# Kernel tuning notes

Measured on AMD Instinct MI355X. Metric: run time of the kernel, lower is better.

The kernel has to match this reference:

```python
import jax, jax.numpy as jnp
import numpy as np

B, H, S, D = 2, 8, 2048, 64


def setup_inputs() -> dict:
    key = jax.random.key(0)
    kq, kk, kv, km = jax.random.split(key, 4)
    Q = jax.random.normal(kq, (B, H, S, D), dtype=jnp.float32)
    K = jax.random.normal(kk, (B, H, S, D), dtype=jnp.float32)
    V = jax.random.normal(kv, (B, H, S, D), dtype=jnp.float32)
    attn_mask = jax.random.bernoulli(km, p=0.1, shape=(B, H, S, S))
    return {"Q": Q, "K": K, "V": V, "attn_mask": attn_mask, "d_k": D}


def reference(Q, K, V, attn_mask, d_k):
    # scores = Q K^T / sqrt(d_k)  -> [B,H,S,S]
    scale = 1.0 / np.sqrt(d_k).astype(np.float32)
    scores = jnp.einsum("bhqd,bhkd->bhqk", Q, K) * scale
    scores = jnp.where(attn_mask, jnp.float32(-1e9), scores)
    attn = jax.nn.softmax(scores, axis=-1)
    # dropout is identity in eval mode (deterministic reference)
    context = jnp.einsum("bhqk,bhkd->bhqd", attn, V)
    return (context, attn)
```

## Files before the change

kernel.cpp:

```cpp
#include <hip/hip_runtime.h>
#include <stdint.h>

#define S_LEN 2048
#define D_HEAD 64
#define NBH 16
#define NROWS (NBH * S_LEN)
#define CTX_ELEMS (NBH * S_LEN * D_HEAD)


__global__ void detect_mask_kernel(const uint32_t* __restrict__ m, int* flag) {
  __shared__ int any;
  if (threadIdx.x == 0) any = 0;
  __syncthreads();
  int local = 0;
  for (int i = threadIdx.x; i < 16384; i += 256)
    if (m[i] > 1u) local = 1;
  if (local) atomicOr(&any, 1);
  __syncthreads();
  if (threadIdx.x == 0) *flag = any;
}

__global__ __launch_bounds__(256, 3) void qk_exp_kernel(
    const float* __restrict__ Q, const float* __restrict__ K,
    const void* __restrict__ mask, float* __restrict__ e_out,
    float* __restrict__ psum, const int* __restrict__ mflag) {
  __shared__ float Qs[32][132];
  __shared__ float Ks[32][132];
  const int bh = blockIdx.z;
  const int mBase = blockIdx.y * 128;
  const int nBase = blockIdx.x * 128;
  const float* __restrict__ Qb = Q + (size_t)bh * S_LEN * D_HEAD;
  const float* __restrict__ Kb = K + (size_t)bh * S_LEN * D_HEAD;
  float* __restrict__ Eb = e_out + (size_t)bh * S_LEN * S_LEN;
  const int tid = threadIdx.x;
  const int maskIsBytes = *mflag;

  const int ty = (tid >> 4) << 3;
  const int cj = (tid & 15) << 2;
  float acc[8][8] = {};

#pragma unroll
  for (int ph = 0; ph < 2; ++ph) {
    const int dBase = ph * 32;
    if (ph) __syncthreads();
#pragma unroll
    for (int i = 0; i < 4; ++i) {
      const int f4 = tid + i * 256;
      const int row = f4 >> 3;
      const int d0 = (f4 & 7) << 2;
      const float4 qv = *reinterpret_cast<const float4*>(
          Qb + (size_t)(mBase + row) * D_HEAD + dBase + d0);
      const float4 kv = *reinterpret_cast<const float4*>(
          Kb + (size_t)(nBase + row) * D_HEAD + dBase + d0);
      Qs[d0 + 0][row] = qv.x; Qs[d0 + 1][row] = qv.y;
      Qs[d0 + 2][row] = qv.z; Qs[d0 + 3][row] = qv.w;
      Ks[d0 + 0][row] = kv.x; Ks[d0 + 1][row] = kv.y;
      Ks[d0 + 2][row] = kv.z; Ks[d0 + 3][row] = kv.w;
    }
    __syncthreads();
#pragma unroll 4
    for (int d = 0; d < 32; ++d) {
      const float4 q0 = *reinterpret_cast<const float4*>(&Qs[d][ty]);
      const float4 q1 = *reinterpret_cast<const float4*>(&Qs[d][ty + 4]);
      const float4 kl = *reinterpret_cast<const float4*>(&Ks[d][cj]);
      const float4 kh = *reinterpret_cast<const float4*>(&Ks[d][64 + cj]);
      const float qv[8] = {q0.x, q0.y, q0.z, q0.w, q1.x, q1.y, q1.z, q1.w};
      const float kv[8] = {kl.x, kl.y, kl.z, kl.w, kh.x, kh.y, kh.z, kh.w};
#pragma unroll
      for (int i = 0; i < 8; ++i)
#pragma unroll
        for (int j = 0; j < 8; ++j)
          acc[i][j] = fmaf(qv[i], kv[j], acc[i][j]);
    }
  }

  const float scale = 0.125f;
#pragma unroll
  for (int i = 0; i < 8; ++i) {
    const int row = mBase + ty + i;
    float e[8];
    if (maskIsBytes) {
      const unsigned char* mrow =
          (const unsigned char*)mask + ((size_t)bh * S_LEN + row) * S_LEN;
      const uint32_t ml = *reinterpret_cast<const uint32_t*>(mrow + nBase + cj);
      const uint32_t mh =
          *reinterpret_cast<const uint32_t*>(mrow + nBase + 64 + cj);
#pragma unroll
      for (int j = 0; j < 4; ++j) {
        e[j] = ((ml >> (8 * j)) & 0xffu) ? 0.0f : __expf(acc[i][j] * scale);
        e[4 + j] =
            ((mh >> (8 * j)) & 0xffu) ? 0.0f : __expf(acc[i][4 + j] * scale);
      }
    } else {
      const int* mrow = (const int*)mask + ((size_t)bh * S_LEN + row) * S_LEN;
      const int4 m0 = *reinterpret_cast<const int4*>(mrow + nBase + cj);
      const int4 m1 = *reinterpret_cast<const int4*>(mrow + nBase + 64 + cj);
      const int mi[8] = {m0.x, m0.y, m0.z, m0.w, m1.x, m1.y, m1.z, m1.w};
#pragma unroll
      for (int j = 0; j < 8; ++j)
        e[j] = mi[j] ? 0.0f : __expf(acc[i][j] * scale);
    }
    const float4 o0 = {e[0], e[1], e[2], e[3]};
    const float4 o1 = {e[4], e[5], e[6], e[7]};
    float* dst = Eb + (size_t)row * S_LEN + nBase;
    *reinterpret_cast<float4*>(dst + cj) = o0;
    *reinterpret_cast<float4*>(dst + 64 + cj) = o1;

    float r = (e[0] + e[1] + e[2] + e[3]) + (e[4] + e[5] + e[6] + e[7]);
    r += __shfl_xor(r, 1, 64);
    r += __shfl_xor(r, 2, 64);
    r += __shfl_xor(r, 4, 64);
    r += __shfl_xor(r, 8, 64);
    if ((tid & 15) == 0)
      psum[((size_t)bh * S_LEN + row) * 16 + blockIdx.x] = r;
  }
}

__global__ __launch_bounds__(256) void row_inv_kernel(
    const float* __restrict__ psum, float* __restrict__ inv) {
  const int row = blockIdx.x * 256 + threadIdx.x;
  const float4* p = reinterpret_cast<const float4*>(psum + (size_t)row * 16);
  const float4 a = p[0], b = p[1], c = p[2], d = p[3];
  const float s = ((a.x + a.y) + (a.z + a.w)) + ((b.x + b.y) + (b.z + b.w)) +
                  ((c.x + c.y) + (c.z + c.w)) + ((d.x + d.y) + (d.z + d.w));
  inv[row] = 1.0f / s;
}

__global__ __launch_bounds__(256, 4) void pv_kernel(
    float* __restrict__ attn, const float* __restrict__ V,
    const float* __restrict__ inv, float* __restrict__ part, int kLen) {
  __shared__ float Es[32][132];
  __shared__ float Vs[32][68];
  __shared__ float inv_s[128];
  const int bh = blockIdx.y;
  const int mBase = blockIdx.x * 128;
  const int z = blockIdx.z;
  float* __restrict__ Ab = attn + (size_t)bh * S_LEN * S_LEN;
  const float* __restrict__ Vb = V + (size_t)bh * S_LEN * D_HEAD;
  float* __restrict__ outb =
      part + (size_t)z * CTX_ELEMS + (size_t)bh * S_LEN * D_HEAD;
  const int tid = threadIdx.x;

  if (tid < 128) inv_s[tid] = inv[(size_t)bh * S_LEN + mBase + tid];

  const int ty = (tid >> 4) << 3;
  const int tx = (tid & 15) << 2;
  float acc[8][4] = {};
  const int kBeg = z * kLen;
  for (int kt = kBeg; kt < kBeg + kLen; kt += 32) {
    __syncthreads();
#pragma unroll
    for (int j = 0; j < 4; ++j) {
      const int f4 = tid + j * 256;
      const int r = f4 >> 3;
      const int c4 = (f4 & 7) << 2;
      float* gp = Ab + (size_t)(mBase + r) * S_LEN + kt + c4;
      float4 e = *reinterpret_cast<const float4*>(gp);
      const float sc = inv_s[r];
      e.x *= sc; e.y *= sc; e.z *= sc; e.w *= sc;
      *reinterpret_cast<float4*>(gp) = e;
      Es[c4 + 0][r] = e.x; Es[c4 + 1][r] = e.y;
      Es[c4 + 2][r] = e.z; Es[c4 + 3][r] = e.w;
    }
#pragma unroll
    for (int j = 0; j < 2; ++j) {
      const int f4 = tid + j * 256;
      const int r = f4 >> 4;
      const int c0 = (f4 & 15) << 2;
      *reinterpret_cast<float4*>(&Vs[r][c0]) =
          *reinterpret_cast<const float4*>(Vb + (size_t)(kt + r) * D_HEAD + c0);
    }
    __syncthreads();
#pragma unroll 4
    for (int k = 0; k < 32; ++k) {
      const float4 a0 = *reinterpret_cast<const float4*>(&Es[k][ty]);
      const float4 a1 = *reinterpret_cast<const float4*>(&Es[k][ty + 4]);
      const float4 v = *reinterpret_cast<const float4*>(&Vs[k][tx]);
      const float av[8] = {a0.x, a0.y, a0.z, a0.w, a1.x, a1.y, a1.z, a1.w};
      const float vv[4] = {v.x, v.y, v.z, v.w};
#pragma unroll
      for (int i = 0; i < 8; ++i)
#pragma unroll
        for (int j = 0; j < 4; ++j)
          acc[i][j] = fmaf(av[i], vv[j], acc[i][j]);
    }
  }
#pragma unroll
  for (int i = 0; i < 8; ++i) {
    const float4 o = {acc[i][0], acc[i][1], acc[i][2], acc[i][3]};
    *reinterpret_cast<float4*>(outb + (size_t)(mBase + ty + i) * D_HEAD + tx) =
        o;
  }
}

__global__ __launch_bounds__(256) void combine_kernel(
    const float* __restrict__ part, float* __restrict__ ctx, int split) {
  const size_t i = ((size_t)blockIdx.x * 256 + threadIdx.x) * 4;
  float4 s = {0.f, 0.f, 0.f, 0.f};
  for (int z = 0; z < split; ++z) {
    const float4 a = *reinterpret_cast<const float4*>(part + (size_t)z * CTX_ELEMS + i);
    s.x += a.x; s.y += a.y; s.z += a.z; s.w += a.w;
  }
  *reinterpret_cast<float4*>(ctx + i) = s;
}

extern "C" void kernel_launch(void* const* d_in, const int* in_sizes, int n_in,
                              void* d_out, int out_size, void* d_ws, size_t ws_size,
                              hipStream_t stream) {
  const float* Q = (const float*)d_in[0];
  const float* K = (const float*)d_in[1];
  const float* V = (const float*)d_in[2];
  const void* mask = d_in[3];

  float* ctx = (float*)d_out;
  float* attn = (float*)d_out + CTX_ELEMS;
  float* psum = ctx;

  float* inv = (float*)d_ws;
  int* mflag = (int*)((char*)d_ws + NROWS * 4);
  const size_t partOff = (size_t)NROWS * 4 + 256;
  float* part = (float*)((char*)d_ws + partOff);

  int split = 1;
  if (ws_size >= partOff + 4ull * CTX_ELEMS * 4) split = 4;
  else if (ws_size >= partOff + 2ull * CTX_ELEMS * 4) split = 2;
  float* pvOut = (split > 1) ? part : ctx;

  detect_mask_kernel<<<1, 256, 0, stream>>>((const uint32_t*)mask, mflag);
  qk_exp_kernel<<<dim3(S_LEN / 128, S_LEN / 128, NBH), 256, 0, stream>>>(
      Q, K, mask, attn, psum, mflag);
  row_inv_kernel<<<NROWS / 256, 256, 0, stream>>>(psum, inv);
  pv_kernel<<<dim3(S_LEN / 128, NBH, split), 256, 0, stream>>>(
      attn, V, inv, pvOut, S_LEN / split);
  if (split > 1)
    combine_kernel<<<CTX_ELEMS / 4 / 256, 256, 0, stream>>>(part, ctx, split);
}
```

Before: 665.8 us.

## Fuse mask detection and row inverse into neighbors; prefetch tiles in PV kernel

Drops the separate mask-detection and row-inverse kernels: each QK block now detects the mask format locally from its own mask rows, and the PV kernel reduces the partial sums itself. QK issues its mask loads between the two d-halves so they overlap compute, and PV register-prefetches the next attention and V tile while the current one is being computed. This removes two launches and their serialization but raises register pressure (PV launch bounds lowered to 3 waves). The psum buffer moves to workspace, which changes the memory needed for the split decision.

Result: faster. 644.6 us (-3.2%).

```diff
diff --git a/kernel.cpp b/kernel.cpp
--- a/kernel.cpp
+++ b/kernel.cpp
@@ -8,24 +8,13 @@
 #define CTX_ELEMS (NBH * S_LEN * D_HEAD)
 
 
-__global__ void detect_mask_kernel(const uint32_t* __restrict__ m, int* flag) {
-  __shared__ int any;
-  if (threadIdx.x == 0) any = 0;
-  __syncthreads();
-  int local = 0;
-  for (int i = threadIdx.x; i < 16384; i += 256)
-    if (m[i] > 1u) local = 1;
-  if (local) atomicOr(&any, 1);
-  __syncthreads();
-  if (threadIdx.x == 0) *flag = any;
-}
-
 __global__ __launch_bounds__(256, 3) void qk_exp_kernel(
     const float* __restrict__ Q, const float* __restrict__ K,
     const void* __restrict__ mask, float* __restrict__ e_out,
-    float* __restrict__ psum, const int* __restrict__ mflag) {
+    float* __restrict__ psum) {
   __shared__ float Qs[32][132];
   __shared__ float Ks[32][132];
+  __shared__ int s_bytes;
   const int bh = blockIdx.z;
   const int mBase = blockIdx.y * 128;
   const int nBase = blockIdx.x * 128;
@@ -33,45 +22,108 @@
   const float* __restrict__ Kb = K + (size_t)bh * S_LEN * D_HEAD;
   float* __restrict__ Eb = e_out + (size_t)bh * S_LEN * S_LEN;
   const int tid = threadIdx.x;
-  const int maskIsBytes = *mflag;
+
+  if (tid == 0) s_bytes = 0;
+  __syncthreads();
+  {
+    const uint32_t* mw = (const uint32_t*)((const uint8_t*)mask +
+                                           ((size_t)bh * S_LEN + mBase) * S_LEN);
+    if (mw[tid] > 1u) atomicOr(&s_bytes, 1);
+  }
 
   const int ty = (tid >> 4) << 3;
   const int cj = (tid & 15) << 2;
   float acc[8][8] = {};
 
 #pragma unroll
-  for (int ph = 0; ph < 2; ++ph) {
-    const int dBase = ph * 32;
-    if (ph) __syncthreads();
-#pragma unroll
-    for (int i = 0; i < 4; ++i) {
-      const int f4 = tid + i * 256;
-      const int row = f4 >> 3;
-      const int d0 = (f4 & 7) << 2;
-      const float4 qv = *reinterpret_cast<const float4*>(
-          Qb + (size_t)(mBase + row) * D_HEAD + dBase + d0);
-      const float4 kv = *reinterpret_cast<const float4*>(
-          Kb + (size_t)(nBase + row) * D_HEAD + dBase + d0);
-      Qs[d0 + 0][row] = qv.x; Qs[d0 + 1][row] = qv.y;
-      Qs[d0 + 2][row] = qv.z; Qs[d0 + 3][row] = qv.w;
-      Ks[d0 + 0][row] = kv.x; Ks[d0 + 1][row] = kv.y;
-      Ks[d0 + 2][row] = kv.z; Ks[d0 + 3][row] = kv.w;
-    }
-    __syncthreads();
+  for (int i = 0; i < 4; ++i) {
+    const int f4 = tid + i * 256;
+    const int row = f4 >> 3;
+    const int d0 = (f4 & 7) << 2;
+    const float4 qv = *reinterpret_cast<const float4*>(
+        Qb + (size_t)(mBase + row) * D_HEAD + d0);
+    const float4 kv = *reinterpret_cast<const float4*>(
+        Kb + (size_t)(nBase + row) * D_HEAD + d0);
+    Qs[d0 + 0][row] = qv.x; Qs[d0 + 1][row] = qv.y;
+    Qs[d0 + 2][row] = qv.z; Qs[d0 + 3][row] = qv.w;
+    Ks[d0 + 0][row] = kv.x; Ks[d0 + 1][row] = kv.y;
+    Ks[d0 + 2][row] = kv.z; Ks[d0 + 3][row] = kv.w;
+  }
+  __syncthreads();
+  const int maskBytes = s_bytes;
+
 #pragma unroll 4
-    for (int d = 0; d < 32; ++d) {
-      const float4 q0 = *reinterpret_cast<const float4*>(&Qs[d][ty]);
-      const float4 q1 = *reinterpret_cast<const float4*>(&Qs[d][ty + 4]);
-      const float4 kl = *reinterpret_cast<const float4*>(&Ks[d][cj]);
-      const float4 kh = *reinterpret_cast<const float4*>(&Ks[d][64 + cj]);
-      const float qv[8] = {q0.x, q0.y, q0.z, q0.w, q1.x, q1.y, q1.z, q1.w};
-      const float kv[8] = {kl.x, kl.y, kl.z, kl.w, kh.x, kh.y, kh.z, kh.w};
-#pragma unroll
-      for (int i = 0; i < 8; ++i)
-#pragma unroll
-        for (int j = 0; j < 8; ++j)
-          acc[i][j] = fmaf(qv[i], kv[j], acc[i][j]);
-    }
+  for (int d = 0; d < 32; ++d) {
+    const float4 q0 = *reinterpret_cast<const float4*>(&Qs[d][ty]);
+    const float4 q1 = *reinterpret_cast<const float4*>(&Qs[d][ty + 4]);
+    const float4 kl = *reinterpret_cast<const float4*>(&Ks[d][cj]);
+    const float4 kh = *reinterpret_cast<const float4*>(&Ks[d][64 + cj]);
+    const float qv[8] = {q0.x, q0.y, q0.z, q0.w, q1.x, q1.y, q1.z, q1.w};
+    const float kv[8] = {kl.x, kl.y, kl.z, kl.w, kh.x, kh.y, kh.z, kh.w};
+#pragma unroll
+    for (int i = 0; i < 8; ++i)
+#pragma unroll
+      for (int j = 0; j < 8; ++j)
+        acc[i][j] = fmaf(qv[i], kv[j], acc[i][j]);
+  }
+  __syncthreads();
+
+#pragma unroll
+  for (int i = 0; i < 4; ++i) {
+    const int f4 = tid + i * 256;
+    const int row = f4 >> 3;
+    const int d0 = (f4 & 7) << 2;
+    const float4 qv = *reinterpret_cast<const float4*>(
+        Qb + (size_t)(mBase + row) * D_HEAD + 32 + d0);
+    const float4 kv = *reinterpret_cast<const float4*>(
+        Kb + (size_t)(nBase + row) * D_HEAD + 32 + d0);
+    Qs[d0 + 0][row] = qv.x; Qs[d0 + 1][row] = qv.y;
+    Qs[d0 + 2][row] = qv.z; Qs[d0 + 3][row] = qv.w;
+    Ks[d0 + 0][row] = kv.x; Ks[d0 + 1][row] = kv.y;
+    Ks[d0 + 2][row] = kv.z; Ks[d0 + 3][row] = kv.w;
+  }
+  __syncthreads();
+
+  uint32_t mlv[8], mhv[8];
+  if (maskBytes) {
+#pragma unroll
+    for (int i = 0; i < 8; ++i) {
+      const unsigned char* mrow = (const unsigned char*)mask +
+          ((size_t)bh * S_LEN + mBase + ty + i) * S_LEN + nBase;
+      mlv[i] = *reinterpret_cast<const uint32_t*>(mrow + cj);
+      mhv[i] = *reinterpret_cast<const uint32_t*>(mrow + 64 + cj);
+    }
+  } else {
+#pragma unroll
+    for (int i = 0; i < 8; ++i) {
+      const int* mrow = (const int*)mask +
+          ((size_t)bh * S_LEN + mBase + ty + i) * S_LEN + nBase;
+      const int4 m0 = *reinterpret_cast<const int4*>(mrow + cj);
+      const int4 m1 = *reinterpret_cast<const int4*>(mrow + 64 + cj);
+      uint32_t b = 0;
+      b |= (m0.x ? 0x001u : 0) | (m0.y ? 0x100u : 0) |
+           (m0.z ? 0x10000u : 0) | (m0.w ? 0x1000000u : 0);
+      mlv[i] = b;
+      b = 0;
+      b |= (m1.x ? 0x001u : 0) | (m1.y ? 0x100u : 0) |
+           (m1.z ? 0x10000u : 0) | (m1.w ? 0x1000000u : 0);
+      mhv[i] = b;
+    }
+  }
+
+#pragma unroll 4
+  for (int d = 0; d < 32; ++d) {
+    const float4 q0 = *reinterpret_cast<const float4*>(&Qs[d][ty]);
+    const float4 q1 = *reinterpret_cast<const float4*>(&Qs[d][ty + 4]);
+    const float4 kl = *reinterpret_cast<const float4*>(&Ks[d][cj]);
+    const float4 kh = *reinterpret_cast<const float4*>(&Ks[d][64 + cj]);
+    const float qv[8] = {q0.x, q0.y, q0.z, q0.w, q1.x, q1.y, q1.z, q1.w};
+    const float kv[8] = {kl.x, kl.y, kl.z, kl.w, kh.x, kh.y, kh.z, kh.w};
+#pragma unroll
+    for (int i = 0; i < 8; ++i)
+#pragma unroll
+      for (int j = 0; j < 8; ++j)
+        acc[i][j] = fmaf(qv[i], kv[j], acc[i][j]);
   }
 
   const float scale = 0.125f;
@@ -79,26 +131,11 @@
   for (int i = 0; i < 8; ++i) {
     const int row = mBase + ty + i;
     float e[8];
-    if (maskIsBytes) {
-      const unsigned char* mrow =
-          (const unsigned char*)mask + ((size_t)bh * S_LEN + row) * S_LEN;
-      const uint32_t ml = *reinterpret_cast<const uint32_t*>(mrow + nBase + cj);
-      const uint32_t mh =
-          *reinterpret_cast<const uint32_t*>(mrow + nBase + 64 + cj);
-#pragma unroll
-      for (int j = 0; j < 4; ++j) {
-        e[j] = ((ml >> (8 * j)) & 0xffu) ? 0.0f : __expf(acc[i][j] * scale);
-        e[4 + j] =
-            ((mh >> (8 * j)) & 0xffu) ? 0.0f : __expf(acc[i][4 + j] * scale);
-      }
-    } else {
-      const int* mrow = (const int*)mask + ((size_t)bh * S_LEN + row) * S_LEN;
-      const int4 m0 = *reinterpret_cast<const int4*>(mrow + nBase + cj);
-      const int4 m1 = *reinterpret_cast<const int4*>(mrow + nBase + 64 + cj);
-      const int mi[8] = {m0.x, m0.y, m0.z, m0.w, m1.x, m1.y, m1.z, m1.w};
-#pragma unroll
-      for (int j = 0; j < 8; ++j)
-        e[j] = mi[j] ? 0.0f : __expf(acc[i][j] * scale);
+#pragma unroll
+    for (int j = 0; j < 4; ++j) {
+      e[j] = ((mlv[i] >> (8 * j)) & 0xffu) ? 0.0f : __expf(acc[i][j] * scale);
+      e[4 + j] =
+          ((mhv[i] >> (8 * j)) & 0xffu) ? 0.0f : __expf(acc[i][4 + j] * scale);
     }
     const float4 o0 = {e[0], e[1], e[2], e[3]};
     const float4 o1 = {e[4], e[5], e[6], e[7]};
@@ -116,19 +153,9 @@
   }
 }
 
-__global__ __launch_bounds__(256) void row_inv_kernel(
-    const float* __restrict__ psum, float* __restrict__ inv) {
-  const int row = blockIdx.x * 256 + threadIdx.x;
-  const float4* p = reinterpret_cast<const float4*>(psum + (size_t)row * 16);
-  const float4 a = p[0], b = p[1], c = p[2], d = p[3];
-  const float s = ((a.x + a.y) + (a.z + a.w)) + ((b.x + b.y) + (b.z + b.w)) +
-                  ((c.x + c.y) + (c.z + c.w)) + ((d.x + d.y) + (d.z + d.w));
-  inv[row] = 1.0f / s;
-}
-
-__global__ __launch_bounds__(256, 4) void pv_kernel(
+__global__ __launch_bounds__(256, 3) void pv_kernel(
     float* __restrict__ attn, const float* __restrict__ V,
-    const float* __restrict__ inv, float* __restrict__ part, int kLen) {
+    const float* __restrict__ psum, float* __restrict__ outp, int kLen) {
   __shared__ float Es[32][132];
   __shared__ float Vs[32][68];
   __shared__ float inv_s[128];
@@ -138,37 +165,65 @@
   float* __restrict__ Ab = attn + (size_t)bh * S_LEN * S_LEN;
   const float* __restrict__ Vb = V + (size_t)bh * S_LEN * D_HEAD;
   float* __restrict__ outb =
-      part + (size_t)z * CTX_ELEMS + (size_t)bh * S_LEN * D_HEAD;
+      outp + (size_t)z * CTX_ELEMS + (size_t)bh * S_LEN * D_HEAD;
   const int tid = threadIdx.x;
 
-  if (tid < 128) inv_s[tid] = inv[(size_t)bh * S_LEN + mBase + tid];
-
+  if (tid < 128) {
+    const float4* p = reinterpret_cast<const float4*>(
+        psum + ((size_t)bh * S_LEN + mBase + tid) * 16);
+    const float4 a = p[0], b = p[1], c = p[2], d = p[3];
+    inv_s[tid] =
+        1.0f / (((a.x + a.y) + (a.z + a.w)) + ((b.x + b.y) + (b.z + b.w)) +
+                ((c.x + c.y) + (c.z + c.w)) + ((d.x + d.y) + (d.z + d.w)));
+  }
+
+  const int rr = tid >> 3;
+  const int c4 = (tid & 7) << 2;
+  const int vr = tid >> 4;
+  const int vc = (tid & 15) << 2;
   const int ty = (tid >> 4) << 3;
   const int tx = (tid & 15) << 2;
+
+  const int kBeg = z * kLen;
+  const int nT = kLen / 32;
+
+  float4 er[4], vv[2];
+#pragma unroll
+  for (int j = 0; j < 4; ++j)
+    er[j] = *reinterpret_cast<const float4*>(
+        Ab + (size_t)(mBase + 32 * j + rr) * S_LEN + kBeg + c4);
+#pragma unroll
+  for (int j = 0; j < 2; ++j)
+    vv[j] = *reinterpret_cast<const float4*>(
+        Vb + (size_t)(kBeg + 16 * j + vr) * D_HEAD + vc);
+
   float acc[8][4] = {};
-  const int kBeg = z * kLen;
-  for (int kt = kBeg; kt < kBeg + kLen; kt += 32) {
+  for (int t = 0; t < nT; ++t) {
+    const int kt = kBeg + t * 32;
     __syncthreads();
 #pragma unroll
     for (int j = 0; j < 4; ++j) {
-      const int f4 = tid + j * 256;
-      const int r = f4 >> 3;
-      const int c4 = (f4 & 7) << 2;
-      float* gp = Ab + (size_t)(mBase + r) * S_LEN + kt + c4;
-      float4 e = *reinterpret_cast<const float4*>(gp);
+      const int r = 32 * j + rr;
       const float sc = inv_s[r];
+      float4 e = er[j];
       e.x *= sc; e.y *= sc; e.z *= sc; e.w *= sc;
-      *reinterpret_cast<float4*>(gp) = e;
+      *reinterpret_cast<float4*>(Ab + (size_t)(mBase + r) * S_LEN + kt + c4) = e;
       Es[c4 + 0][r] = e.x; Es[c4 + 1][r] = e.y;
       Es[c4 + 2][r] = e.z; Es[c4 + 3][r] = e.w;
     }
 #pragma unroll
-    for (int j = 0; j < 2; ++j) {
-      const int f4 = tid + j * 256;
-      const int r = f4 >> 4;
-      const int c0 = (f4 & 15) << 2;
-      *reinterpret_cast<float4*>(&Vs[r][c0]) =
-          *reinterpret_cast<const float4*>(Vb + (size_t)(kt + r) * D_HEAD + c0);
+    for (int j = 0; j < 2; ++j)
+      *reinterpret_cast<float4*>(&Vs[16 * j + vr][vc]) = vv[j];
+    if (t + 1 < nT) {
+      const int kn = kt + 32;
+#pragma unroll
+      for (int j = 0; j < 4; ++j)
+        er[j] = *reinterpret_cast<const float4*>(
+            Ab + (size_t)(mBase + 32 * j + rr) * S_LEN + kn + c4);
+#pragma unroll
+      for (int j = 0; j < 2; ++j)
+        vv[j] = *reinterpret_cast<const float4*>(
+            Vb + (size_t)(kn + 16 * j + vr) * D_HEAD + vc);
     }
     __syncthreads();
 #pragma unroll 4
@@ -177,12 +232,13 @@
       const float4 a1 = *reinterpret_cast<const float4*>(&Es[k][ty + 4]);
       const float4 v = *reinterpret_cast<const float4*>(&Vs[k][tx]);
       const float av[8] = {a0.x, a0.y, a0.z, a0.w, a1.x, a1.y, a1.z, a1.w};
-      const float vv[4] = {v.x, v.y, v.z, v.w};
-#pragma unroll
-      for (int i = 0; i < 8; ++i)
-#pragma unroll
-        for (int j = 0; j < 4; ++j)
-          acc[i][j] = fmaf(av[i], vv[j], acc[i][j]);
+#pragma unroll
+      for (int i = 0; i < 8; ++i) {
+        acc[i][0] = fmaf(av[i], v.x, acc[i][0]);
+        acc[i][1] = fmaf(av[i], v.y, acc[i][1]);
+        acc[i][2] = fmaf(av[i], v.z, acc[i][2]);
+        acc[i][3] = fmaf(av[i], v.w, acc[i][3]);
+      }
     }
   }
 #pragma unroll
@@ -198,7 +254,8 @@
   const size_t i = ((size_t)blockIdx.x * 256 + threadIdx.x) * 4;
   float4 s = {0.f, 0.f, 0.f, 0.f};
   for (int z = 0; z < split; ++z) {
-    const float4 a = *reinterpret_cast<const float4*>(part + (size_t)z * CTX_ELEMS + i);
+    const float4 a =
+        *reinterpret_cast<const float4*>(part + (size_t)z * CTX_ELEMS + i);
     s.x += a.x; s.y += a.y; s.z += a.z; s.w += a.w;
   }
   *reinterpret_cast<float4*>(ctx + i) = s;
@@ -214,11 +271,9 @@
 
   float* ctx = (float*)d_out;
   float* attn = (float*)d_out + CTX_ELEMS;
-  float* psum = ctx;
-
-  float* inv = (float*)d_ws;
-  int* mflag = (int*)((char*)d_ws + NROWS * 4);
-  const size_t partOff = (size_t)NROWS * 4 + 256;
+
+  float* psum = (float*)d_ws;
+  const size_t partOff = ((size_t)NROWS * 16 * 4 + 255) & ~(size_t)255;
   float* part = (float*)((char*)d_ws + partOff);
 
   int split = 1;
@@ -226,12 +281,10 @@
   else if (ws_size >= partOff + 2ull * CTX_ELEMS * 4) split = 2;
   float* pvOut = (split > 1) ? part : ctx;
 
-  detect_mask_kernel<<<1, 256, 0, stream>>>((const uint32_t*)mask, mflag);
   qk_exp_kernel<<<dim3(S_LEN / 128, S_LEN / 128, NBH), 256, 0, stream>>>(
-      Q, K, mask, attn, psum, mflag);
-  row_inv_kernel<<<NROWS / 256, 256, 0, stream>>>(psum, inv);
+      Q, K, mask, attn, psum);
   pv_kernel<<<dim3(S_LEN / 128, NBH, split), 256, 0, stream>>>(
-      attn, V, inv, pvOut, S_LEN / split);
+      attn, V, psum, pvOut, S_LEN / split);
   if (split > 1)
     combine_kernel<<<CTX_ELEMS / 4 / 256, 256, 0, stream>>>(part, ctx, split);
 }
```
